# Optimization experiments

Measured on AMD Instinct MI355X. Metric: run time of the kernel, lower is better.

## Reference

```python
import jax, jax.numpy as jnp
import numpy as np

B, N, K, D, F, H = 8, 512, 16, 256, 1024, 8


def _ln(x, g, b):
    m = jnp.mean(x, axis=-1, keepdims=True)
    v = jnp.var(x, axis=-1, keepdims=True)
    return (x - m) / jnp.sqrt(v + 1e-5) * g + b


def _mlp(x, W1, b1, W2, b2):
    return jax.nn.gelu(x @ W1 + b1, approximate=False) @ W2 + b2


def setup_inputs() -> dict:
    key = jax.random.key(0)
    ks = jax.random.split(key, 16)
    s = 0.02
    inp = {
        'x': jax.random.normal(ks[0], (N, B, D), jnp.float32),
        'e': jax.random.normal(ks[1], (B, N, K, D), jnp.float32),
        'edge_index': jax.random.randint(ks[2], (B, N, K), 0, N),
        'Wq': jax.random.normal(ks[3], (D, D), jnp.float32) * s,
        'bq': jnp.zeros((D,), jnp.float32),
        'Wk': jax.random.normal(ks[4], (D, D), jnp.float32) * s,
        'bk': jnp.zeros((D,), jnp.float32),
        'Wv': jax.random.normal(ks[5], (D, D), jnp.float32) * s,
        'bv': jnp.zeros((D,), jnp.float32),
        'Wo': jax.random.normal(ks[6], (D, D), jnp.float32) * s,
        'bo': jnp.zeros((D,), jnp.float32),
        'nW1': jax.random.normal(ks[7], (D, F), jnp.float32) * s,
        'nb1': jnp.zeros((F,), jnp.float32),
        'nW2': jax.random.normal(ks[8], (F, D), jnp.float32) * s,
        'nb2': jnp.zeros((D,), jnp.float32),
        'eW1': jax.random.normal(ks[9], (D, F), jnp.float32) * s,
        'eb1': jnp.zeros((F,), jnp.float32),
        'eW2': jax.random.normal(ks[10], (F, D), jnp.float32) * s,
        'eb2': jnp.zeros((D,), jnp.float32),
        'na_g': jnp.ones((D,), jnp.float32), 'na_b': jnp.zeros((D,), jnp.float32),
        'ea_g': jnp.ones((D,), jnp.float32), 'ea_b': jnp.zeros((D,), jnp.float32),
        'nf_g': jnp.ones((D,), jnp.float32), 'nf_b': jnp.zeros((D,), jnp.float32),
        'ef_g': jnp.ones((D,), jnp.float32), 'ef_b': jnp.zeros((D,), jnp.float32),
    }
    return inp


def reference(x, e, edge_index, Wq, bq, Wk, bk, Wv, bv, Wo, bo,
              nW1, nb1, nW2, nb2, eW1, eb1, eW2, eb2,
              na_g, na_b, ea_g, ea_b, nf_g, nf_b, ef_g, ef_b):
    n, b, d = x.shape
    hd = d // H
    xt = jnp.transpose(x, (1, 0, 2))  # (B, N, D) residual in batch-first layout
    bi = jnp.arange(b)[:, None, None]
    ni = jnp.arange(n)[None, :, None]

    # scatter edge features into dense additive attention bias (B, N, N)
    attn_bias = jnp.zeros((b, n, n), x.dtype).at[bi, ni, edge_index].set(e.mean(-1))

    def heads(t):  # (B,N,D) -> (B,H,N,hd)
        return t.reshape(b, n, H, hd).transpose(0, 2, 1, 3)

    q = heads(xt @ Wq + bq) * (hd ** -0.5)
    k = heads(xt @ Wk + bk)
    v = heads(xt @ Wv + bv)
    logits = jnp.einsum('bhnd,bhmd->bhnm', q, k) + attn_bias[:, None]
    attn = jax.nn.softmax(logits, axis=-1)  # (B,H,N,N)
    out = jnp.einsum('bhnm,bhmd->bhnd', attn, v)
    out = out.transpose(0, 2, 1, 3).reshape(b, n, d) @ Wo + bo

    xn = _ln(xt + out, na_g, na_b)  # (B,N,D)

    # edge update: gather attn weights and neighbor node features via edge_index
    weights = attn.mean(axis=1)  # (B,N,N) head-averaged
    w = weights[bi, edge_index, ni]  # (B,N,K): weights[b, edge_index[b,n,k], n]
    gathered = xt[jnp.arange(b)[:, None, None], edge_index]  # (B,N,K,D)
    e2 = _ln(e + w[..., None] * gathered, ea_g, ea_b)

    xn = _ln(xn + _mlp(xn, nW1, nb1, nW2, nb2), nf_g, nf_b)
    e2 = _ln(e2 + _mlp(e2, eW1, eb1, eW2, eb2), ef_g, ef_b)
    return jnp.transpose(xn, (1, 0, 2)), e2
```

## Files before the change

### kernel.cpp

```cpp
#include <hip/hip_runtime.h>
#include <hip/hip_bf16.h>
#include <hip/hip_fp8.h>
#include <math.h>

#define B_ 8
#define N_ 512
#define K_ 16
#define D_ 256
#define F_ 1024
#define H_ 8
#define HD_ 32
#define M_ (B_*N_)
#define R_ (B_*N_*K_)

typedef __bf16 bf16x8 __attribute__((ext_vector_type(8)));
typedef float  f32x4  __attribute__((ext_vector_type(4)));

__device__ inline short bf16s(float f) {
    __hip_bfloat16 h = __float2bfloat16(f);
    return *reinterpret_cast<short*>(&h);
}
__device__ inline float b2f(short s) {
    union { float f; unsigned u; } v; v.u = ((unsigned)(unsigned short)s) << 16; return v.f;
}
__device__ inline unsigned char f8e4m3(float f) {
    union { __hip_fp8_e4m3 h; unsigned char c; } u;
    u.h = __hip_fp8_e4m3(f);
    return u.c;
}

__device__ __forceinline__ void gload16(const void* g, void* l) {
    __builtin_amdgcn_global_load_lds(
        (const __attribute__((address_space(1))) unsigned int*)g,
        (__attribute__((address_space(3))) unsigned int*)l, 16, 0, 0);
}

__global__ __launch_bounds__(256) void transposeAll(
        const float* __restrict__ Wq, const float* __restrict__ Wk,
        const float* __restrict__ Wv, const float* __restrict__ Wo,
        const float* __restrict__ nW1, const float* __restrict__ nW2,
        const float* __restrict__ eW1, const float* __restrict__ eW2,
        short* __restrict__ WqkvT, short* __restrict__ WoT,
        short* __restrict__ nW1T, short* __restrict__ nW2T,
        short* __restrict__ eW1T, unsigned char* __restrict__ eW2T8)
{
    const float* W; short* WT = nullptr; int Kk, Nn; float sc = 1.f;
    switch (blockIdx.z) {
        case 0: W=Wq;  WT=WqkvT;          Kk=256;  Nn=256;  sc=0.17677669529663687f; break;
        case 1: W=Wk;  WT=WqkvT+256*256;  Kk=256;  Nn=256;  break;
        case 2: W=Wv;  WT=WqkvT+512*256;  Kk=256;  Nn=256;  break;
        case 3: W=Wo;  WT=WoT;            Kk=256;  Nn=256;  break;
        case 4: W=nW1; WT=nW1T;           Kk=256;  Nn=1024; break;
        case 5: W=nW2; WT=nW2T;           Kk=1024; Nn=256;  break;
        case 6: W=eW1; WT=eW1T;           Kk=256;  Nn=1024; break;
        default:W=eW2;                    Kk=1024; Nn=256;  break;
    }
    const int bx = blockIdx.x, by = blockIdx.y;
    if (bx >= Nn/32 || by >= Kk/32) return;
    __shared__ float tile[32][33];
    int tx = threadIdx.x & 31, ty = threadIdx.x >> 5;
    #pragma unroll
    for (int j = 0; j < 4; ++j) {
        int k = by*32 + ty + j*8;
        tile[ty + j*8][tx] = W[(size_t)k*Nn + bx*32 + tx];
    }
    __syncthreads();
    if (blockIdx.z == 7) {
        #pragma unroll
        for (int j = 0; j < 4; ++j) {
            int n = bx*32 + ty + j*8;
            eW2T8[(size_t)n*Kk + by*32 + tx] = f8e4m3(tile[tx][ty + j*8] * 64.f);
        }
    } else {
        #pragma unroll
        for (int j = 0; j < 4; ++j) {
            int n = bx*32 + ty + j*8;
            WT[(size_t)n*Kk + by*32 + tx] = bf16s(tile[tx][ty + j*8] * sc);
        }
    }
}

__global__ __launch_bounds__(256) void build_bqkv(const float* __restrict__ bq,
        const float* __restrict__ bk, const float* __restrict__ bv,
        float* __restrict__ bqkv)
{
    int t = blockIdx.x*256 + threadIdx.x;
    if (t >= 768) return;
    float v = (t < 256) ? bq[t]*0.17677669529663687f
            : (t < 512) ? bk[t-256] : bv[t-512];
    bqkv[t] = v;
}

__global__ __launch_bounds__(256) void conv_x(const float* __restrict__ x,
        short* __restrict__ xtb)
{
    int row = blockIdx.x;
    int d = threadIdx.x;
    int b = row >> 9, n = row & 511;
    xtb[(size_t)row*D_ + d] = bf16s(x[((size_t)n*B_ + b)*D_ + d]);
}

__global__ __launch_bounds__(256) void edge_means(const float* __restrict__ e,
        float* __restrict__ means)
{
    long row = (long)blockIdx.x*4 + (threadIdx.x >> 6);
    int lane = threadIdx.x & 63;
    float4 v = ((const float4*)(e + row*D_))[lane];
    float s = v.x + v.y + v.z + v.w;
    for (int o = 1; o < 64; o <<= 1) s += __shfl_xor(s, o);
    if (lane == 0) means[row] = s * (1.f/D_);
}

__global__ __launch_bounds__(256) void bias_build(const int* __restrict__ ei,
        const float* __restrict__ means, float* __restrict__ biasb)
{
    const int r0 = blockIdx.x * 16;
    float4* bp4 = (float4*)(biasb + (size_t)r0*N_);
    #pragma unroll
    for (int i = threadIdx.x; i < 16*N_/4; i += 256)
        bp4[i] = make_float4(0.f, 0.f, 0.f, 0.f);
    __syncthreads();
    if (threadIdx.x < 16) {
        const int idx = r0 + threadIdx.x;
        const int* ep = ei + (size_t)idx*K_;
        const float* mp = means + (size_t)idx*K_;
        float* bp = biasb + (size_t)idx*N_;
        for (int k = 0; k < K_; ++k) bp[ep[k]] = mp[k];
    }
}

__global__ __launch_bounds__(256) void gemm_qkv(
        const short* __restrict__ A, const short* __restrict__ BT,
        const float* __restrict__ bias, short* __restrict__ Cb,
        short* __restrict__ vtb, int Kk)
{
    __shared__ __align__(16) short As[128*32];
    __shared__ __align__(16) short Bs[128*32];
    const int t = threadIdx.x;
    const int lane = t & 63;
    const int wave = t >> 6;
    const int wr = (wave >> 1) * 64;
    const int wc = (wave & 1) * 64;
    const int bm = blockIdx.x, bn = blockIdx.y;
    f32x4 acc[4][4] = {};
    const int srow = lane >> 2;
    const int sk   = (lane & 3) * 8;
    const int fr = lane & 15;
    const int fk = (lane >> 4) * 8;
    for (int k0 = 0; k0 < Kk; k0 += 32) {
        __syncthreads();
        #pragma unroll
        for (int i = 0; i < 2; ++i) {
            const int rb = wave*16 + i*64;
            gload16(A  + (size_t)(bm*128 + rb + srow)*Kk + k0 + sk, &As[rb*32]);
            gload16(BT + (size_t)(bn*128 + rb + srow)*Kk + k0 + sk, &Bs[rb*32]);
        }
        __syncthreads();
        bf16x8 af[4], bfr[4];
        #pragma unroll
        for (int i2 = 0; i2 < 4; ++i2)
            af[i2] = *(const bf16x8*)&As[(wr + i2*16 + fr)*32 + fk];
        #pragma unroll
        for (int n2 = 0; n2 < 4; ++n2)
            bfr[n2] = *(const bf16x8*)&Bs[(wc + n2*16 + fr)*32 + fk];
        #pragma unroll
        for (int i2 = 0; i2 < 4; ++i2)
            #pragma unroll
            for (int n2 = 0; n2 < 4; ++n2)
                acc[i2][n2] = __builtin_amdgcn_mfma_f32_16x16x32_bf16(
                        af[i2], bfr[n2], acc[i2][n2], 0, 0, 0);
    }
    const int fq4 = (lane >> 4) * 4;
    #pragma unroll
    for (int i2 = 0; i2 < 4; ++i2) {
        #pragma unroll
        for (int n2 = 0; n2 < 4; ++n2) {
            const int col = bn*128 + wc + n2*16 + fr;
            const float bv = bias[col];
            const int rowb = bm*128 + wr + i2*16 + fq4;
            if (col < 512) {
                #pragma unroll
                for (int r2 = 0; r2 < 4; ++r2)
                    Cb[(size_t)(rowb + r2)*512 + col] = bf16s(acc[i2][n2][r2] + bv);
            } else {
                const int b = rowb >> 9, n = rowb & 511;
                const int dv = col - 512, h = dv >> 5, dh = dv & 31;
                short4 s4;
                s4.x = bf16s(acc[i2][n2][0] + bv);
                s4.y = bf16s(acc[i2][n2][1] + bv);
                s4.z = bf16s(acc[i2][n2][2] + bv);
                s4.w = bf16s(acc[i2][n2][3] + bv);
                *(short4*)&vtb[((size_t)((b*H_ + h)*HD_ + dh))*512 + n] = s4;
            }
        }
    }
}

template<bool F8>
__global__ __launch_bounds__(512, 4) void gemm_gelu(
        const short* __restrict__ A, const short* __restrict__ BT,
        const float* __restrict__ bias, short* __restrict__ Cb,
        unsigned char* __restrict__ C8, int Nn, int Kk)
{
    __shared__ __align__(16) short As[2][128*32];
    __shared__ __align__(16) short Bs[2][256*32];
    const int t = threadIdx.x;
    const int lane = t & 63;
    const int wave = t >> 6;
    const int wrg = (wave >> 2) * 64;
    const int wc  = (wave & 3) * 64;
    const int bm = blockIdx.x, bn = blockIdx.y;
    f32x4 acc[4][4] = {};
    const int srow = lane >> 2;
    const int sk   = (lane & 3) * 8;
    const int fr = lane & 15;
    const int fk = (lane >> 4) * 8;
    auto stage = [&](int s, int k0) {
        {
            const int rb = wave*16;
            gload16(A + (size_t)(bm*128 + rb + srow)*Kk + k0 + sk, &As[s][rb*32]);
        }
        #pragma unroll
        for (int i = 0; i < 2; ++i) {
            const int rb = wave*16 + i*128;
            gload16(BT + (size_t)(bn*256 + rb + srow)*Kk + k0 + sk, &Bs[s][rb*32]);
        }
    };
    stage(0, 0);
    __syncthreads();
    int cur = 0;
    for (int k0 = 0; k0 < Kk; k0 += 32) {
        if (k0 + 32 < Kk) stage(cur ^ 1, k0 + 32);
        bf16x8 af[4], bfr[4];
        #pragma unroll
        for (int i2 = 0; i2 < 4; ++i2)
            af[i2] = *(const bf16x8*)&As[cur][(wrg + i2*16 + fr)*32 + fk];
        #pragma unroll
        for (int n2 = 0; n2 < 4; ++n2)
            bfr[n2] = *(const bf16x8*)&Bs[cur][(wc + n2*16 + fr)*32 + fk];
        #pragma unroll
        for (int i2 = 0; i2 < 4; ++i2)
            #pragma unroll
            for (int n2 = 0; n2 < 4; ++n2)
                acc[i2][n2] = __builtin_amdgcn_mfma_f32_16x16x32_bf16(
                        af[i2], bfr[n2], acc[i2][n2], 0, 0, 0);
        __syncthreads();
        cur ^= 1;
    }
    const int fq4 = (lane >> 4) * 4;
    #pragma unroll
    for (int i2 = 0; i2 < 4; ++i2) {
        #pragma unroll
        for (int n2 = 0; n2 < 4; ++n2) {
            const int col = bn*256 + wc + n2*16 + fr;
            const float bv = bias[col];
            #pragma unroll
            for (int r2 = 0; r2 < 4; ++r2) {
                const int row = bm*128 + wrg + i2*16 + fq4 + r2;
                float v = acc[i2][n2][r2] + bv;
                v = 0.5f*v*(1.f + erff(v*0.70710678118654752f));
                if constexpr (F8) C8[(size_t)row*Nn + col] = f8e4m3(v * 16.f);
                else              Cb[(size_t)row*Nn + col] = bf16s(v);
            }
        }
    }
}

template<bool TRANSOUT, int RESMODE, bool DUALOUT>
__global__ __launch_bounds__(512, 4) void gemm_ln2(
        const short* __restrict__ A, const short* __restrict__ BT,
        const float* __restrict__ bias, const float* __restrict__ resf,
        const short* __restrict__ resb,
        const float* __restrict__ g, const float* __restrict__ bt,
        float* __restrict__ out, short* __restrict__ outb, int Kk)
{
    __shared__ __align__(16) short As[2][128*32];
    __shared__ __align__(16) short Bs[2][256*32];
    __shared__ float rs[128][4][2];
    __shared__ float mr[128][2];
    const int t = threadIdx.x;
    const int lane = t & 63;
    const int wave = t >> 6;
    const int wrg = (wave >> 2) * 64;
    const int wc  = (wave & 3) * 64;
    const int bm = blockIdx.x;
    f32x4 acc[4][4] = {};
    const int srow = lane >> 2;
    const int sk   = (lane & 3) * 8;
    const int fr = lane & 15;
    const int fk = (lane >> 4) * 8;
    auto stage = [&](int s, int k0) {
        {
            const int rb = wave*16;
            gload16(A + (size_t)(bm*128 + rb + srow)*Kk + k0 + sk, &As[s][rb*32]);
        }
        #pragma unroll
        for (int i = 0; i < 2; ++i) {
            const int rb = wave*16 + i*128;
            gload16(BT + (size_t)(rb + srow)*Kk + k0 + sk, &Bs[s][rb*32]);
        }
    };
    stage(0, 0);
    __syncthreads();
    int cur = 0;
    for (int k0 = 0; k0 < Kk; k0 += 32) {
        if (k0 + 32 < Kk) stage(cur ^ 1, k0 + 32);
        bf16x8 af[4], bfr[4];
        #pragma unroll
        for (int i2 = 0; i2 < 4; ++i2)
            af[i2] = *(const bf16x8*)&As[cur][(wrg + i2*16 + fr)*32 + fk];
        #pragma unroll
        for (int n2 = 0; n2 < 4; ++n2)
            bfr[n2] = *(const bf16x8*)&Bs[cur][(wc + n2*16 + fr)*32 + fk];
        #pragma unroll
        for (int i2 = 0; i2 < 4; ++i2)
            #pragma unroll
            for (int n2 = 0; n2 < 4; ++n2)
                acc[i2][n2] = __builtin_amdgcn_mfma_f32_16x16x32_bf16(
                        af[i2], bfr[n2], acc[i2][n2], 0, 0, 0);
        __syncthreads();
        cur ^= 1;
    }
    const int fq4 = (lane >> 4) * 4;
    float ps[4][4] = {}, pq[4][4] = {};
    #pragma unroll
    for (int i2 = 0; i2 < 4; ++i2) {
        #pragma unroll
        for (int n2 = 0; n2 < 4; ++n2) {
            const int c = wc + n2*16 + fr;
            const float bv = bias[c];
            #pragma unroll
            for (int r2 = 0; r2 < 4; ++r2) {
                const int row = wrg + i2*16 + fq4 + r2;
                const size_t grow = (size_t)bm*128 + row;
                float rv;
                if constexpr (RESMODE == 1) rv = b2f(resb[grow*256 + c]);
                else if constexpr (RESMODE == 2) {
                    const int bb = (int)(grow >> 9), nn = (int)(grow & 511);
                    rv = resf[((size_t)nn*B_ + bb)*256 + c];
                } else rv = resf[grow*256 + c];
                float v = acc[i2][n2][r2] + bv + rv;
                acc[i2][n2][r2] = v;
                ps[i2][r2] += v;
                pq[i2][r2] += v*v;
            }
        }
    }
    #pragma unroll
    for (int i2 = 0; i2 < 4; ++i2)
        #pragma unroll
        for (int r2 = 0; r2 < 4; ++r2)
            #pragma unroll
            for (int o = 1; o < 16; o <<= 1) {
                ps[i2][r2] += __shfl_xor(ps[i2][r2], o);
                pq[i2][r2] += __shfl_xor(pq[i2][r2], o);
            }
    if ((lane & 15) == 0) {
        #pragma unroll
        for (int i2 = 0; i2 < 4; ++i2)
            #pragma unroll
            for (int r2 = 0; r2 < 4; ++r2) {
                const int row = wrg + i2*16 + fq4 + r2;
                rs[row][wave & 3][0] = ps[i2][r2];
                rs[row][wave & 3][1] = pq[i2][r2];
            }
    }
    __syncthreads();
    if (t < 128) {
        float S = 0.f, Q = 0.f;
        #pragma unroll
        for (int w = 0; w < 4; ++w) { S += rs[t][w][0]; Q += rs[t][w][1]; }
        const float mean = S * (1.f/D_);
        mr[t][0] = mean;
        mr[t][1] = rsqrtf(Q * (1.f/D_) - mean*mean + 1e-5f);
    }
    __syncthreads();
    #pragma unroll
    for (int i2 = 0; i2 < 4; ++i2) {
        #pragma unroll
        for (int n2 = 0; n2 < 4; ++n2) {
            const int c = wc + n2*16 + fr;
            const float gv = g[c], bv2 = bt[c];
            #pragma unroll
            for (int r2 = 0; r2 < 4; ++r2) {
                const int row = wrg + i2*16 + fq4 + r2;
                const size_t grow = (size_t)bm*128 + row;
                const float o = (acc[i2][n2][r2] - mr[row][0])*mr[row][1]*gv + bv2;
                if constexpr (TRANSOUT) {
                    const int bb = (int)(grow >> 9), nn = (int)(grow & 511);
                    out[((size_t)nn*B_ + bb)*D_ + c] = o;
                } else {
                    out[grow*256 + c] = o;
                }
                if constexpr (DUALOUT)
                    outb[grow*256 + c] = bf16s(o);
            }
        }
    }
}

__global__ __launch_bounds__(512, 4) void gemm_ln2f8(
        const unsigned char* __restrict__ A, const unsigned char* __restrict__ BT,
        const float* __restrict__ bias, const short* __restrict__ resb,
        const float* __restrict__ g, const float* __restrict__ bt,
        float* __restrict__ out)
{
    __shared__ __align__(16) unsigned char As[2][128*64];
    __shared__ __align__(16) unsigned char Bs[2][256*64];
    __shared__ float rs[128][4][2];
    __shared__ float mr[128][2];
    const int t = threadIdx.x;
    const int lane = t & 63;
    const int wave = t >> 6;
    const int wrg = (wave >> 2) * 64;
    const int wc  = (wave & 3) * 64;
    const int bm = blockIdx.x;
    f32x4 acc[4][4] = {};
    const int srow = lane >> 2;
    const int skb  = (lane & 3) * 16;
    const int fr  = lane & 15;
    const int fk8 = (lane >> 4) * 8;
    auto stage = [&](int s, int k0) {
        {
            const int rb = wave*16;
            gload16(A + (size_t)(bm*128 + rb + srow)*1024 + k0 + skb, &As[s][rb*64]);
        }
        #pragma unroll
        for (int i = 0; i < 2; ++i) {
            const int rb = wave*16 + i*128;
            gload16(BT + (size_t)(rb + srow)*1024 + k0 + skb, &Bs[s][rb*64]);
        }
    };
    stage(0, 0);
    __syncthreads();
    int cur = 0;
    for (int k0 = 0; k0 < 1024; k0 += 64) {
        if (k0 + 64 < 1024) stage(cur ^ 1, k0 + 64);
        long a8[2][4], b8[2][4];
        #pragma unroll
        for (int s = 0; s < 2; ++s) {
            #pragma unroll
            for (int i2 = 0; i2 < 4; ++i2)
                a8[s][i2] = *(const long*)&As[cur][(wrg + i2*16 + fr)*64 + s*32 + fk8];
            #pragma unroll
            for (int n2 = 0; n2 < 4; ++n2)
                b8[s][n2] = *(const long*)&Bs[cur][(wc + n2*16 + fr)*64 + s*32 + fk8];
        }
        #pragma unroll
        for (int s = 0; s < 2; ++s)
            #pragma unroll
            for (int i2 = 0; i2 < 4; ++i2)
                #pragma unroll
                for (int n2 = 0; n2 < 4; ++n2)
                    acc[i2][n2] = __builtin_amdgcn_mfma_f32_16x16x32_fp8_fp8(
                            a8[s][i2], b8[s][n2], acc[i2][n2], 0, 0, 0);
        __syncthreads();
        cur ^= 1;
    }
    const int fq4 = (lane >> 4) * 4;
    float ps[4][4] = {}, pq[4][4] = {};
    #pragma unroll
    for (int i2 = 0; i2 < 4; ++i2) {
        #pragma unroll
        for (int n2 = 0; n2 < 4; ++n2) {
            const int c = wc + n2*16 + fr;
            const float bv = bias[c];
            #pragma unroll
            for (int r2 = 0; r2 < 4; ++r2) {
                const int row = wrg + i2*16 + fq4 + r2;
                const size_t grow = (size_t)bm*128 + row;
                float v = acc[i2][n2][r2]*(1.f/1024.f) + bv + b2f(resb[grow*256 + c]);
                acc[i2][n2][r2] = v;
                ps[i2][r2] += v;
                pq[i2][r2] += v*v;
            }
        }
    }
    #pragma unroll
    for (int i2 = 0; i2 < 4; ++i2)
        #pragma unroll
        for (int r2 = 0; r2 < 4; ++r2)
            #pragma unroll
            for (int o = 1; o < 16; o <<= 1) {
                ps[i2][r2] += __shfl_xor(ps[i2][r2], o);
                pq[i2][r2] += __shfl_xor(pq[i2][r2], o);
            }
    if ((lane & 15) == 0) {
        #pragma unroll
        for (int i2 = 0; i2 < 4; ++i2)
            #pragma unroll
            for (int r2 = 0; r2 < 4; ++r2) {
                const int row = wrg + i2*16 + fq4 + r2;
                rs[row][wave & 3][0] = ps[i2][r2];
                rs[row][wave & 3][1] = pq[i2][r2];
            }
    }
    __syncthreads();
    if (t < 128) {
        float S = 0.f, Q = 0.f;
        #pragma unroll
        for (int w = 0; w < 4; ++w) { S += rs[t][w][0]; Q += rs[t][w][1]; }
        const float mean = S * (1.f/D_);
        mr[t][0] = mean;
        mr[t][1] = rsqrtf(Q * (1.f/D_) - mean*mean + 1e-5f);
    }
    __syncthreads();
    #pragma unroll
    for (int i2 = 0; i2 < 4; ++i2) {
        #pragma unroll
        for (int n2 = 0; n2 < 4; ++n2) {
            const int c = wc + n2*16 + fr;
            const float gv = g[c], bv2 = bt[c];
            #pragma unroll
            for (int r2 = 0; r2 < 4; ++r2) {
                const int row = wrg + i2*16 + fq4 + r2;
                const size_t grow = (size_t)bm*128 + row;
                out[grow*256 + c] = (acc[i2][n2][r2] - mr[row][0])*mr[row][1]*gv + bv2;
            }
        }
    }
}

__global__ __launch_bounds__(256) void attn_fused(const short* __restrict__ qkb,
        const short* __restrict__ vtb, const float* __restrict__ biasb,
        float* __restrict__ rowsum, short* __restrict__ actx)
{
    __shared__ __align__(16) short Qs[128*32];
    __shared__ __align__(16) short Ks[128*32];
    __shared__ __align__(16) short Vs[32*128];
    __shared__ __align__(16) short Ps[128*128];
    const int it = blockIdx.x, bh = blockIdx.y;
    const int b = bh >> 3, h = bh & 7;
    const int t = threadIdx.x;
    const int lane = t & 63;
    const int wave = t >> 6;
    const int wr0 = wave * 32;
    const int srow = lane >> 2;
    const int sk   = (lane & 3) * 8;
    const int srow8 = lane >> 4;
    const int ck16  = lane & 15;
    const int fr = lane & 15;
    const int fk = (lane >> 4) * 8;
    const int fq4 = (lane >> 4) * 4;
    const int I0 = it * 128;
    #pragma unroll
    for (int i = 0; i < 2; ++i) {
        const int rb = wave*16 + i*64;
        gload16(qkb + (size_t)(b*N_ + I0 + rb + srow)*512 + h*HD_ + sk, &Qs[rb*32]);
    }
    float rsum[2][4] = {};
    f32x4 apv[2][2] = {};
    const float LOG2E = 1.4426950408889634f;
    for (int jt = 0; jt < 4; ++jt) {
        const int J0 = jt * 128;
        __syncthreads();
        #pragma unroll
        for (int i = 0; i < 2; ++i) {
            const int rb = wave*16 + i*64;
            gload16(qkb + (size_t)(b*N_ + J0 + rb + srow)*512 + 256 + h*HD_ + sk, &Ks[rb*32]);
        }
        #pragma unroll
        for (int i = 0; i < 2; ++i) {
            const int db = wave*8 + i*4;
            const int dh = db + srow8;
            gload16(vtb + ((size_t)bh*HD_ + dh)*512 + J0 + ((ck16 ^ (dh & 7)) * 8),
                    &Vs[db*128]);
        }
        __syncthreads();
        bf16x8 aq[2], kf8[8];
        #pragma unroll
        for (int i2 = 0; i2 < 2; ++i2)
            aq[i2] = *(const bf16x8*)&Qs[(wr0 + i2*16 + fr)*32 + fk];
        #pragma unroll
        for (int n2 = 0; n2 < 8; ++n2)
            kf8[n2] = *(const bf16x8*)&Ks[(n2*16 + fr)*32 + fk];
        #pragma unroll
        for (int i2 = 0; i2 < 2; ++i2) {
            #pragma unroll
            for (int n2 = 0; n2 < 8; ++n2) {
                f32x4 z = {0.f, 0.f, 0.f, 0.f};
                f32x4 s = __builtin_amdgcn_mfma_f32_16x16x32_bf16(aq[i2], kf8[n2], z, 0, 0, 0);
                const int jg = J0 + n2*16 + fr;
                #pragma unroll
                for (int r2 = 0; r2 < 4; ++r2) {
                    const int rloc = wr0 + i2*16 + fq4 + r2;
                    const float l = s[r2] + biasb[((size_t)b*N_ + I0 + rloc)*N_ + jg];
                    const float p = exp2f(fminf(l, 80.f) * LOG2E);
                    rsum[i2][r2] += p;
                    int idx = rloc*128 + n2*16 + fr;
                    idx ^= (rloc & 7) << 3;
                    Ps[idx] = bf16s(p);
                }
            }
        }
        __syncthreads();
        #pragma unroll
        for (int ks = 0; ks < 4; ++ks) {
            bf16x8 ap[2], bv[2];
            #pragma unroll
            for (int i2 = 0; i2 < 2; ++i2) {
                const int r = wr0 + i2*16 + fr;
                int idx = r*128 + ks*32 + fk;
                idx ^= (r & 7) << 3;
                ap[i2] = *(const bf16x8*)&Ps[idx];
            }
            #pragma unroll
            for (int n2 = 0; n2 < 2; ++n2) {
                const int dh = n2*16 + fr;
                const int q = lane >> 4;
                const int slot = (ks*4 + q) ^ (dh & 7);
                bv[n2] = *(const bf16x8*)&Vs[dh*128 + slot*8];
            }
            #pragma unroll
            for (int i2 = 0; i2 < 2; ++i2)
                #pragma unroll
                for (int n2 = 0; n2 < 2; ++n2)
                    apv[i2][n2] = __builtin_amdgcn_mfma_f32_16x16x32_bf16(
                            ap[i2], bv[n2], apv[i2][n2], 0, 0, 0);
        }
    }
    #pragma unroll
    for (int i2 = 0; i2 < 2; ++i2)
        #pragma unroll
        for (int r2 = 0; r2 < 4; ++r2)
            #pragma unroll
            for (int o = 1; o < 16; o <<= 1)
                rsum[i2][r2] += __shfl_xor(rsum[i2][r2], o);
    #pragma unroll
    for (int i2 = 0; i2 < 2; ++i2) {
        #pragma unroll
        for (int r2 = 0; r2 < 4; ++r2) {
            const int row = wr0 + i2*16 + fq4 + r2;
            if (fr == 0)
                rowsum[(size_t)bh*N_ + I0 + row] = rsum[i2][r2];
            const float inv = 1.f / rsum[i2][r2];
            #pragma unroll
            for (int n2 = 0; n2 < 2; ++n2)
                actx[((size_t)b*N_ + I0 + row)*D_ + h*HD_ + n2*16 + fr]
                    = bf16s(apv[i2][n2][r2] * inv);
        }
    }
}

__device__ inline void ln_core(float v[4], int lane, const float* __restrict__ g,
        const float* __restrict__ bt, float out[4])
{
    float s  = v[0] + v[1] + v[2] + v[3];
    float sq = v[0]*v[0] + v[1]*v[1] + v[2]*v[2] + v[3]*v[3];
    for (int o = 1; o < 64; o <<= 1) { s += __shfl_xor(s, o); sq += __shfl_xor(sq, o); }
    float mean = s * (1.f/D_);
    float rstd = rsqrtf(sq * (1.f/D_) - mean*mean + 1e-5f);
    const float4 gv = *(const float4*)(g  + lane*4);
    const float4 bv = *(const float4*)(bt + lane*4);
    out[0] = (v[0]-mean)*rstd*gv.x + bv.x;
    out[1] = (v[1]-mean)*rstd*gv.y + bv.y;
    out[2] = (v[2]-mean)*rstd*gv.z + bv.z;
    out[3] = (v[3]-mean)*rstd*gv.w + bv.w;
}

__global__ __launch_bounds__(256) void edge_update(const float* __restrict__ e,
        const float* __restrict__ x, const int* __restrict__ ei,
        const short* __restrict__ qkb, const float* __restrict__ biasb,
        const float* __restrict__ rowsum, const float* __restrict__ g,
        const float* __restrict__ bt, short* __restrict__ e2b)
{
    long row = (long)blockIdx.x*4 + (threadIdx.x >> 6);
    int lane = threadIdx.x & 63;
    long bi = row >> 4;
    long b = bi / N_; int i = (int)(bi % N_);
    int ej = ei[row];
    const short4 q4 = *(const short4*)(qkb + ((size_t)b*N_ + ej)*512 + lane*4);
    const short4 k4 = *(const short4*)(qkb + ((size_t)b*N_ + i)*512 + 256 + lane*4);
    float dot = b2f(q4.x)*b2f(k4.x) + b2f(q4.y)*b2f(k4.y)
              + b2f(q4.z)*b2f(k4.z) + b2f(q4.w)*b2f(k4.w);
    dot += __shfl_xor(dot, 1); dot += __shfl_xor(dot, 2); dot += __shfl_xor(dot, 4);
    const int h = lane >> 3;
    const float l = dot + biasb[((size_t)b*N_ + ej)*N_ + i];
    float p = exp2f(fminf(l, 80.f) * 1.4426950408889634f)
            / rowsum[((size_t)b*H_ + h)*N_ + ej];
    p += __shfl_xor(p, 8); p += __shfl_xor(p, 16); p += __shfl_xor(p, 32);
    const float w = p * (1.f/H_);
    const float4 ev = *(const float4*)(e + row*D_ + lane*4);
    const float4 xv = *(const float4*)(x + ((size_t)ej*B_ + b)*D_ + lane*4);
    float v[4] = {ev.x + w*xv.x, ev.y + w*xv.y, ev.z + w*xv.z, ev.w + w*xv.w};
    float o[4];
    ln_core(v, lane, g, bt, o);
    short4 s4; s4.x = bf16s(o[0]); s4.y = bf16s(o[1]); s4.z = bf16s(o[2]); s4.w = bf16s(o[3]);
    *(short4*)(e2b + row*D_ + lane*4) = s4;
}

extern "C" void kernel_launch(void* const* d_in, const int* in_sizes, int n_in,
                              void* d_out, int out_size, void* d_ws, size_t ws_size,
                              hipStream_t stream)
{
    (void)in_sizes; (void)n_in; (void)out_size; (void)ws_size;
    const float* x    = (const float*)d_in[0];
    const float* e    = (const float*)d_in[1];
    const int*   ei   = (const int*)d_in[2];
    const float* Wq   = (const float*)d_in[3];
    const float* bq   = (const float*)d_in[4];
    const float* Wk   = (const float*)d_in[5];
    const float* bk   = (const float*)d_in[6];
    const float* Wv   = (const float*)d_in[7];
    const float* bv   = (const float*)d_in[8];
    const float* Wo   = (const float*)d_in[9];
    const float* bo   = (const float*)d_in[10];
    const float* nW1  = (const float*)d_in[11];
    const float* nb1  = (const float*)d_in[12];
    const float* nW2  = (const float*)d_in[13];
    const float* nb2  = (const float*)d_in[14];
    const float* eW1  = (const float*)d_in[15];
    const float* eb1  = (const float*)d_in[16];
    const float* eW2  = (const float*)d_in[17];
    const float* eb2  = (const float*)d_in[18];
    const float* na_g = (const float*)d_in[19];
    const float* na_b = (const float*)d_in[20];
    const float* ea_g = (const float*)d_in[21];
    const float* ea_b = (const float*)d_in[22];
    const float* nf_g = (const float*)d_in[23];
    const float* nf_b = (const float*)d_in[24];
    const float* ef_g = (const float*)d_in[25];
    const float* ef_b = (const float*)d_in[26];

    float* out1 = (float*)d_out;
    float* e2f  = out1 + (size_t)N_*B_*D_;

    char* wp = (char*)d_ws;
    auto alloc = [&](size_t bytes) -> char* {
        char* p = wp; wp += (bytes + 255) & ~(size_t)255; return p;
    };
    short* WqkvT  = (short*)alloc((size_t)768*D_*2);
    float* bqkv   = (float*)alloc(768*4);
    short* WoT    = (short*)alloc((size_t)D_*D_*2);
    short* nW1T   = (short*)alloc((size_t)F_*D_*2);
    short* nW2T   = (short*)alloc((size_t)D_*F_*2);
    short* eW1T   = (short*)alloc((size_t)F_*D_*2);
    unsigned char* eW2T8 = (unsigned char*)alloc((size_t)D_*F_);
    float* rowsum = (float*)alloc((size_t)B_*H_*N_*4);
    short* e2b    = (short*)alloc((size_t)R_*D_*2);
    char* ov = wp;
    auto allocA = [&](size_t bytes) -> char* {
        char* p = ov; ov += (bytes + 255) & ~(size_t)255; return p;
    };
    short* xtb    = (short*)allocA((size_t)M_*D_*2);
    float* means  = (float*)allocA((size_t)R_*4);
    float* biasb  = (float*)allocA((size_t)B_*N_*N_*4);
    short* qkb    = (short*)allocA((size_t)M_*512*2);
    short* vtb    = (short*)allocA((size_t)B_*H_*HD_*N_*2);
    short* actx   = (short*)allocA((size_t)M_*D_*2);
    float* xn     = (float*)allocA((size_t)M_*D_*4);
    short* xnb    = (short*)allocA((size_t)M_*D_*2);
    short* nhid   = (short*)allocA((size_t)M_*F_*2);
    unsigned char* ehid8 = (unsigned char*)wp;

    transposeAll<<<dim3(32, 32, 8), 256, 0, stream>>>(Wq, Wk, Wv, Wo,
            nW1, nW2, eW1, eW2, WqkvT, WoT, nW1T, nW2T, eW1T, eW2T8);
    build_bqkv<<<3, 256, 0, stream>>>(bq, bk, bv, bqkv);
    conv_x<<<M_, 256, 0, stream>>>(x, xtb);

    edge_means<<<R_/4, 256, 0, stream>>>(e, means);
    bias_build<<<M_/16, 256, 0, stream>>>(ei, means, biasb);

    gemm_qkv<<<dim3(M_/128, 768/128), 256, 0, stream>>>(
            xtb, WqkvT, bqkv, qkb, vtb, D_);

    attn_fused<<<dim3(N_/128, B_*H_), 256, 0, stream>>>(qkb, vtb, biasb, rowsum, actx);

    gemm_ln2<false,2,true><<<M_/128, 512, 0, stream>>>(
            actx, WoT, bo, x, nullptr, na_g, na_b, xn, xnb, D_);

    gemm_gelu<false><<<dim3(M_/128, F_/256), 512, 0, stream>>>(
            xnb, nW1T, nb1, nhid, nullptr, F_, D_);
    gemm_ln2<true,0,false><<<M_/128, 512, 0, stream>>>(
            nhid, nW2T, nb2, xn, nullptr, nf_g, nf_b, out1, nullptr, F_);

    edge_update<<<R_/4, 256, 0, stream>>>(e, x, ei, qkb, biasb, rowsum,
            ea_g, ea_b, e2b);
    gemm_gelu<true><<<dim3(R_/128, F_/256), 512, 0, stream>>>(
            e2b, eW1T, eb1, nullptr, ehid8, F_, D_);
    gemm_ln2f8<<<R_/128, 512, 0, stream>>>(
            ehid8, eW2T8, eb2, e2b, ef_g, ef_b, e2f);
}
```

Baseline: 356.6 us.

## Swizzle FP8 GEMM operand layout so LDS fragments load as 16-byte vectors

Stores the FP8 GELU hidden activations and the transposed eW2 weights in a permuted, XOR-swizzled byte order within each 64-wide K chunk. Each lane's two 8-byte MFMA k-slices then sit next to each other and can be read from LDS with one 16-byte load instead of two 8-byte loads. The XOR on the row index is meant to spread those reads across LDS banks. Producer kernels and the consumer GEMM must agree on the permutation, and the global stores of the producers become scattered within each 64-byte chunk.

```diff
diff --git a/kernel.cpp b/kernel.cpp
--- a/kernel.cpp
+++ b/kernel.cpp
@@ -15,6 +15,7 @@
 
 typedef __bf16 bf16x8 __attribute__((ext_vector_type(8)));
 typedef float  f32x4  __attribute__((ext_vector_type(4)));
+typedef long   i64x2  __attribute__((ext_vector_type(2)));
 
 __device__ inline short bf16s(float f) {
     __hip_bfloat16 h = __float2bfloat16(f);
@@ -27,6 +28,9 @@
     union { __hip_fp8_e4m3 h; unsigned char c; } u;
     u.h = __hip_fp8_e4m3(f);
     return u.c;
+}
+__device__ __forceinline__ int f8pos(int w, int row) {
+    return ((((w >> 3) & 3) ^ (row & 3)) << 4) | ((w >> 5) << 3) | (w & 7);
 }
 
 __device__ __forceinline__ void gload16(const void* g, void* l) {
@@ -69,7 +73,10 @@
         #pragma unroll
         for (int j = 0; j < 4; ++j) {
             int n = bx*32 + ty + j*8;
-            eW2T8[(size_t)n*Kk + by*32 + tx] = f8e4m3(tile[tx][ty + j*8] * 64.f);
+            int k = by*32 + tx;
+            int c = k >> 6, w = k & 63;
+            eW2T8[(size_t)n*1024 + (c<<6) + f8pos(w, n)] =
+                f8e4m3(tile[tx][ty + j*8] * 64.f);
         }
     } else {
         #pragma unroll
@@ -259,8 +266,12 @@
                 const int row = bm*128 + wrg + i2*16 + fq4 + r2;
                 float v = acc[i2][n2][r2] + bv;
                 v = 0.5f*v*(1.f + erff(v*0.70710678118654752f));
-                if constexpr (F8) C8[(size_t)row*Nn + col] = f8e4m3(v * 16.f);
-                else              Cb[(size_t)row*Nn + col] = bf16s(v);
+                if constexpr (F8) {
+                    const int c = col >> 6, w = col & 63;
+                    C8[(size_t)row*1024 + (c<<6) + f8pos(w, row)] = f8e4m3(v * 16.f);
+                } else {
+                    Cb[(size_t)row*Nn + col] = bf16s(v);
+                }
             }
         }
     }
@@ -418,8 +429,8 @@
     f32x4 acc[4][4] = {};
     const int srow = lane >> 2;
     const int skb  = (lane & 3) * 16;
-    const int fr  = lane & 15;
-    const int fk8 = (lane >> 4) * 8;
+    const int fr = lane & 15;
+    const int q16 = (lane >> 4);
     auto stage = [&](int s, int k0) {
         {
             const int rb = wave*16;
@@ -438,13 +449,16 @@
         if (k0 + 64 < 1024) stage(cur ^ 1, k0 + 64);
         long a8[2][4], b8[2][4];
         #pragma unroll
-        for (int s = 0; s < 2; ++s) {
-            #pragma unroll
-            for (int i2 = 0; i2 < 4; ++i2)
-                a8[s][i2] = *(const long*)&As[cur][(wrg + i2*16 + fr)*64 + s*32 + fk8];
-            #pragma unroll
-            for (int n2 = 0; n2 < 4; ++n2)
-                b8[s][n2] = *(const long*)&Bs[cur][(wc + n2*16 + fr)*64 + s*32 + fk8];
+        for (int i2 = 0; i2 < 4; ++i2) {
+            const int ar = wrg + i2*16 + fr;
+            const i64x2 av = *(const i64x2*)&As[cur][ar*64 + ((q16 ^ (ar & 3)) << 4)];
+            a8[0][i2] = av[0]; a8[1][i2] = av[1];
+        }
+        #pragma unroll
+        for (int n2 = 0; n2 < 4; ++n2) {
+            const int br = wc + n2*16 + fr;
+            const i64x2 bv = *(const i64x2*)&Bs[cur][br*64 + ((q16 ^ (br & 3)) << 4)];
+            b8[0][n2] = bv[0]; b8[1][n2] = bv[1];
         }
         #pragma unroll
         for (int s = 0; s < 2; ++s)
```

After: 319.1 us. -10.5%, faster.
